# Performance work log

Measured on AMD Instinct MI355X. Metric: run time of the kernel, lower is better.

The kernel has to match this reference:

```python
import jax, jax.numpy as jnp
import numpy as np

B, T, D, H = 2, 2048, 1024, 16
HD = D // H
REG = 16
WIN = 256
ROPE_BASE = 10000.0


def _rope_cos_sin(t, hd):
    theta = 1.0 / (ROPE_BASE ** (jnp.arange(0, hd, 2, dtype=jnp.float32) / hd))  # [hd/2]
    idx_theta = jnp.arange(t, dtype=jnp.float32)[:, None] * theta[None, :]       # [T, hd/2]
    return jnp.cos(idx_theta), jnp.sin(idx_theta)


def _apply_rope(x, cos, sin):
    # x: [B, T, H, HD]
    xs = x.reshape(*x.shape[:-1], HD // 2, 2)
    x0, x1 = xs[..., 0], xs[..., 1]
    c = cos[None, :, None, :]
    s = sin[None, :, None, :]
    out = jnp.stack([x0 * c - x1 * s, x1 * c + x0 * s], axis=-1)
    return out.reshape(x.shape)


def _keep_mask(t):
    # Faithful to _build_attention_register_mask: True = attend (SDPA bool semantics).
    i = jnp.arange(t)[:, None]
    j = jnp.arange(t)[None, :]
    half = WIN // 2
    window_block = (i >= REG) & (j >= jnp.maximum(REG, i - half)) & (j <= i + half)
    blocked = (j < REG) | (i < REG) | window_block
    return ~blocked  # [T, T] bool


def setup_inputs() -> dict:
    key = jax.random.key(0)
    k1, k2, k3 = jax.random.split(key, 3)
    x = jax.random.normal(k1, (B, T, D), dtype=jnp.float32)
    w_attn = jax.random.normal(k2, (3 * D, D), dtype=jnp.float32) * 0.02  # torch Linear weight [out,in]
    w_proj = jax.random.normal(k3, (D, D), dtype=jnp.float32) * 0.02
    return {"x": x, "w_attn": w_attn, "w_proj": w_proj}


def reference(x, w_attn, w_proj):
    b, t, d = x.shape
    qkv = jnp.einsum('btd,ed->bte', x, w_attn)               # [B,T,3D]
    q, k, v = jnp.split(qkv, 3, axis=-1)
    q = q.reshape(b, t, H, HD)
    k = k.reshape(b, t, H, HD)
    v = v.reshape(b, t, H, HD)
    cos, sin = _rope_cos_sin(t, HD)
    q = _apply_rope(q, cos, sin)
    k = _apply_rope(k, cos, sin)
    q = q.transpose(0, 2, 1, 3)  # [B,H,T,HD]
    k = k.transpose(0, 2, 1, 3)
    v = v.transpose(0, 2, 1, 3)
    keep = _keep_mask(t)
    scores = jnp.einsum('bhqd,bhkd->bhqk', q, k) / jnp.sqrt(jnp.float32(HD))
    scores = jnp.where(keep[None, None], scores, -jnp.inf)
    # safe softmax (fully-masked rows -> 0, matching SDPA efficient backends)
    m = jnp.max(scores, axis=-1, keepdims=True)
    m = jnp.where(jnp.isfinite(m), m, 0.0)
    e = jnp.exp(scores - m)
    s = jnp.sum(e, axis=-1, keepdims=True)
    probs = e / jnp.maximum(s, 1e-20)
    y = jnp.einsum('bhqk,bhkd->bhqd', probs, v)
    y = y.transpose(0, 2, 1, 3).reshape(b, t, d)
    return jnp.einsum('btd,ed->bte', y, w_proj)
```

## Files before the change

kernel.cpp:

```cpp
#include <hip/hip_runtime.h>
#include <hip/hip_bf16.h>

#define DEV static __device__ __forceinline__

typedef __attribute__((ext_vector_type(8))) short bf16x8;
typedef __attribute__((ext_vector_type(4))) short bf16x4;
typedef __attribute__((ext_vector_type(4))) float f32x4;

#define MFMA16(a, b, c) __builtin_amdgcn_mfma_f32_16x16x32_bf16((a), (b), (c), 0, 0, 0)

DEV f32x4 pv_mfma(bf16x4 a, bf16x4 b, f32x4 c) {
#if __has_builtin(__builtin_amdgcn_mfma_f32_16x16x16_bf16)
  return __builtin_amdgcn_mfma_f32_16x16x16_bf16(a, b, c, 0, 0, 0);
#elif __has_builtin(__builtin_amdgcn_mfma_f32_16x16x16bf16_1k)
  return __builtin_amdgcn_mfma_f32_16x16x16bf16_1k(a, b, c, 0, 0, 0);
#else
  f32x4 d;
  asm volatile("v_mfma_f32_16x16x16_bf16 %0, %1, %2, %3"
               : "=v"(d) : "v"(a), "v"(b), "v"(c));
  return d;
#endif
}

#define B_ 2
#define T_ 2048
#define D_ 1024
#define H_ 16
#define HD_ 64
#define LOG2E 1.4426950408889634f

DEV short f2bf(float f) {
  union { float f; unsigned u; } w; w.f = f;
  unsigned u = w.u + 0x7fffu + ((w.u >> 16) & 1u);
  return (short)(u >> 16);
}

DEV void gld16(const void* g, void* l) {
  __builtin_amdgcn_global_load_lds(
      (const __attribute__((address_space(1))) void*)g,
      (__attribute__((address_space(3))) void*)l, 16, 0, 0);
}

#define XN 4194304
#define WAN 3145728
__global__ void cvt_k(const float* __restrict__ x, const float* __restrict__ wa,
                      const float* __restrict__ wp, short* __restrict__ xb,
                      short* __restrict__ wab, short* __restrict__ wpb) {
  size_t gi = ((size_t)blockIdx.x * 256 + threadIdx.x) * 8;
  const float* src; short* dst;
  if (gi < XN) { src = x + gi; dst = xb + gi; }
  else if (gi < XN + WAN) { src = wa + (gi - XN); dst = wab + (gi - XN); }
  else { src = wp + (gi - XN - WAN); dst = wpb + (gi - XN - WAN); }
  float4 a = *(const float4*)src;
  float4 b = *(const float4*)(src + 4);
  bf16x8 o;
  o[0] = f2bf(a.x); o[1] = f2bf(a.y); o[2] = f2bf(a.z); o[3] = f2bf(a.w);
  o[4] = f2bf(b.x); o[5] = f2bf(b.y); o[6] = f2bf(b.z); o[7] = f2bf(b.w);
  *(bf16x8*)dst = o;
}

__global__ void rope_table_k(float2* __restrict__ tab) {
  int i = blockIdx.x * 256 + threadIdx.x;
  if (i >= T_ * 32) return;
  int t = i >> 5, d = i & 31;
  float theta = powf(10000.0f, -(float)(2 * d) / 64.0f);
  float a = (float)t * theta;
  tab[i] = make_float2(cosf(a), sinf(a));
}

#define GEMM_CORE(Aptr, Bptr, KDIM)                                              \
  __shared__ short aT[128 * 64];                                                 \
  __shared__ short bT[128 * 64];                                                 \
  const int tid = threadIdx.x;                                                   \
  const int lane = tid & 63, w = tid >> 6;                                       \
  const int l15 = lane & 15, lg = lane >> 4;                                     \
  const int wr = w >> 1, wc = w & 1;                                             \
  const int mBase = blockIdx.y * 128, nBase = blockIdx.x * 128;                  \
  const int lrow = lane >> 3;                                                    \
  const int gch = (lane & 7) ^ lrow;                                             \
  const short* Asrc = (Aptr) + (size_t)(mBase + w * 32 + lrow) * (KDIM) + gch * 8;\
  const short* Bsrc = (Bptr) + (size_t)(nBase + w * 32 + lrow) * (KDIM) + gch * 8;\
  short* aDst = aT + w * 2048;                                                   \
  short* bDst = bT + w * 2048;                                                   \
  f32x4 acc[4][4];                                                               \
  _Pragma("unroll") for (int i = 0; i < 4; ++i)                                  \
  _Pragma("unroll") for (int j = 0; j < 4; ++j)                                  \
      acc[i][j] = (f32x4){0.f, 0.f, 0.f, 0.f};                                   \
  const int nk = (KDIM) / 64;                                                    \
  for (int kt = 0; kt < nk; ++kt) {                                              \
    if (kt) __syncthreads();                                                     \
    _Pragma("unroll") for (int p = 0; p < 4; ++p) {                              \
      gld16(Asrc + kt * 64 + p * 8 * (KDIM), aDst + p * 512);                    \
      gld16(Bsrc + kt * 64 + p * 8 * (KDIM), bDst + p * 512);                    \
    }                                                                            \
    __syncthreads();                \
    bf16x8 af[4][2], bfv[4][2];                                                  \
    _Pragma("unroll") for (int i = 0; i < 4; ++i)                                \
    _Pragma("unroll") for (int s = 0; s < 2; ++s) {                              \
      const int ra = wr * 64 + i * 16 + l15;                                     \
      const int rb = wc * 64 + i * 16 + l15;                                     \
      af[i][s] = *(const bf16x8*)&aT[ra * 64 + (((4 * s + lg) ^ (ra & 7)) * 8)]; \
      bfv[i][s] = *(const bf16x8*)&bT[rb * 64 + (((4 * s + lg) ^ (rb & 7)) * 8)];\
    }                                                                            \
    _Pragma("unroll") for (int mi = 0; mi < 4; ++mi)                             \
    _Pragma("unroll") for (int ni = 0; ni < 4; ++ni)                             \
    _Pragma("unroll") for (int s = 0; s < 2; ++s)                                \
        acc[mi][ni] = MFMA16(af[mi][s], bfv[ni][s], acc[mi][ni]);                \
  }

__global__ void gemm_qkv_k(const short* __restrict__ Xb, const short* __restrict__ Wb,
                           short* __restrict__ Q, short* __restrict__ Ko,
                           short* __restrict__ Vt, const float2* __restrict__ tab) {
  GEMM_CORE(Xb, Wb, 1024)

  const int sec = nBase >> 10;
#pragma unroll
  for (int mi = 0; mi < 4; ++mi) {
    const int m0 = mBase + wr * 64 + mi * 16 + lg * 4;
#pragma unroll
    for (int ni = 0; ni < 4; ++ni) {
      const int n = nBase + wc * 64 + ni * 16 + l15;
      const int hd = n & 63;
      const int h = (n >> 6) & 15;
      if (sec < 2) {
        short* dst = (sec == 0) ? Q : Ko;
        const float qscale = (sec == 0) ? (0.125f * LOG2E) : 1.0f;
#pragma unroll
        for (int r = 0; r < 4; ++r) {
          int m = m0 + r; int b = m >> 11; int t = m & 2047;
          float v = acc[mi][ni][r];
          float pv = __shfl_xor(v, 1);
          float2 cs = tab[t * 32 + (hd >> 1)];
          float o = (lane & 1) ? (v * cs.x + pv * cs.y) : (v * cs.x - pv * cs.y);
          o *= qscale;
          dst[(((size_t)b * H_ + h) * T_ + t) * HD_ + hd] = f2bf(o);
        }
      } else {
        int b = m0 >> 11; int t0 = m0 & 2047;
        short4 s4;
        s4.x = f2bf(acc[mi][ni][0]); s4.y = f2bf(acc[mi][ni][1]);
        s4.z = f2bf(acc[mi][ni][2]); s4.w = f2bf(acc[mi][ni][3]);
        *(short4*)&Vt[(((size_t)b * H_ + h) * HD_ + hd) * T_ + t0] = s4;
      }
    }
  }
}

__global__ __launch_bounds__(256, 4) void attn_k(const short* __restrict__ Qg,
                                                 const short* __restrict__ Kg,
                                                 const short* __restrict__ Vg,
                                                 short* __restrict__ Y) {
  __shared__ short kLds[64 * 72];
  __shared__ short vLds[64 * 72];
  const int tid = threadIdx.x;
  const int lane = tid & 63, w = tid >> 6;
  const int l15 = lane & 15, lg = lane >> 4;
  const int bid = blockIdx.x;
  const int wg = ((bid & 7) << 7) | (bid >> 3);
  const int qt = wg & 31, bh = wg >> 5;
  const int b = bh >> 4, h = bh & 15;
  const int q0 = qt * 64;
  const short* Qh = Qg + (size_t)bh * T_ * HD_;
  const short* Kh = Kg + (size_t)bh * T_ * HD_;
  const short* Vh = Vg + (size_t)bh * HD_ * T_;

  bf16x8 qb[2];
  {
    const int qrow = q0 + w * 16 + l15;
    qb[0] = *(const bf16x8*)&Qh[(size_t)qrow * HD_ + lg * 8];
    qb[1] = *(const bf16x8*)&Qh[(size_t)qrow * HD_ + 32 + lg * 8];
  }
  f32x4 ot[4];
#pragma unroll
  for (int i = 0; i < 4; ++i) ot[i] = (f32x4){0.f, 0.f, 0.f, 0.f};
  float lsum = 0.f;

  const int sRow = tid >> 3, sC = (tid & 7) * 8;
  bf16x8 kreg[2], vreg[2];
  auto issueLoad = [&](int kt) {
    const int k0 = kt * 64;
#pragma unroll
    for (int p = 0; p < 2; ++p) {
      const int row = sRow + p * 32;
      kreg[p] = *(const bf16x8*)&Kh[(size_t)(k0 + row) * HD_ + sC];
      vreg[p] = *(const bf16x8*)&Vh[(size_t)row * T_ + k0 + sC];
    }
  };
  auto inBand = [&](int kt) { const int k0 = kt * 64; return k0 >= q0 - 65 && k0 <= q0 + 65; };

  const int NT = T_ / 64;
  int kt = 0;
  while (kt < NT && inBand(kt)) ++kt;
  issueLoad(kt);

  while (kt < NT) {
    int ktn = kt + 1;
    while (ktn < NT && inBand(ktn)) ++ktn;

    __syncthreads();
#pragma unroll
    for (int p = 0; p < 2; ++p) {
      const int row = sRow + p * 32;
      *(bf16x8*)&kLds[row * 72 + (((tid & 7) ^ (row & 7)) * 8)] = kreg[p];
      *(bf16x8*)&vLds[row * 72 + sC] = vreg[p];
    }
    if (ktn < NT) issueLoad(ktn);
    asm volatile("s_waitcnt lgkmcnt(0)" ::: "memory");
    __builtin_amdgcn_s_barrier();

    const int k0 = kt * 64;
    const bool clean = (q0 >= 16) && (k0 >= 16) &&
                       ((k0 + 63 < q0 - 128) || (k0 > q0 + 63 + 128));

    f32x4 s[4];
#pragma unroll
    for (int i = 0; i < 4; ++i) s[i] = (f32x4){0.f, 0.f, 0.f, 0.f};
    __builtin_amdgcn_s_setprio(1);
#pragma unroll
    for (int nf = 0; nf < 4; ++nf)
#pragma unroll
      for (int ks = 0; ks < 2; ++ks) {
        const int row = nf * 16 + l15;
        bf16x8 ka = *(const bf16x8*)&kLds[row * 72 + (((ks * 4 + lg) ^ (row & 7)) * 8)];
        s[nf] = MFMA16(ka, qb[ks], s[nf]);
      }
    __builtin_amdgcn_s_setprio(0);

    const int i_q = q0 + w * 16 + l15;
    bf16x4 pf[4];
#pragma unroll
    for (int nf = 0; nf < 4; ++nf)
#pragma unroll
      for (int r = 0; r < 4; ++r) {
        if (!clean) {
          const int j = k0 + nf * 16 + lg * 4 + r;
          const bool keep = (i_q >= 16) && (j >= 16) &&
                            ((j < i_q - 128) || (j > i_q + 128));
          if (!keep) s[nf][r] = -__builtin_inff();
        }
        float e = __builtin_amdgcn_exp2f(s[nf][r]);
        lsum += e;
        pf[nf][r] = f2bf(e);
      }

    __builtin_amdgcn_s_setprio(1);
#pragma unroll
    for (int kk = 0; kk < 4; ++kk) {
      bf16x4 va[4];
#pragma unroll
      for (int dt = 0; dt < 4; ++dt)
        va[dt] = *(const bf16x4*)&vLds[(dt * 16 + l15) * 72 + kk * 16 + lg * 4];
#pragma unroll
      for (int dt = 0; dt < 4; ++dt)
        ot[dt] = pv_mfma(va[dt], pf[kk], ot[dt]);
    }
    __builtin_amdgcn_s_setprio(0);
    kt = ktn;
  }

  float l = lsum;
  l += __shfl_xor(l, 16);
  l += __shfl_xor(l, 32);
  const float rl = 1.0f / fmaxf(l, 1e-20f);

  __syncthreads();
  short* tl = kLds + w * (16 * 72);
#pragma unroll
  for (int dt = 0; dt < 4; ++dt) {
    short4 s4;
    s4.x = f2bf(ot[dt][0] * rl);
    s4.y = f2bf(ot[dt][1] * rl);
    s4.z = f2bf(ot[dt][2] * rl);
    s4.w = f2bf(ot[dt][3] * rl);
    *(short4*)&tl[l15 * 72 + dt * 16 + lg * 4] = s4;
  }
  const int rr = lane >> 3, cc = (lane & 7) * 8;
#pragma unroll
  for (int hf = 0; hf < 2; ++hf) {
    const int row = hf * 8 + rr;
    bf16x8 v = *(const bf16x8*)&tl[row * 72 + cc];
    const int t = q0 + w * 16 + row;
    *(bf16x8*)&Y[((size_t)(b * T_ + t)) * D_ + h * HD_ + cc] = v;
  }
}

__global__ void gemm_proj_k(const short* __restrict__ Yg, const short* __restrict__ Wb,
                            float* __restrict__ Out) {
  GEMM_CORE(Yg, Wb, 1024)

#pragma unroll
  for (int mi = 0; mi < 4; ++mi)
#pragma unroll
    for (int ni = 0; ni < 4; ++ni)
#pragma unroll
      for (int r = 0; r < 4; ++r)
        Out[(size_t)(mBase + wr * 64 + mi * 16 + lg * 4 + r) * 1024 +
            nBase + wc * 64 + ni * 16 + l15] = acc[mi][ni][r];
}

extern "C" void kernel_launch(void* const* d_in, const int* in_sizes, int n_in,
                              void* d_out, int out_size, void* d_ws, size_t ws_size,
                              hipStream_t stream) {
  const float* x = (const float*)d_in[0];
  const float* w_attn = (const float*)d_in[1];
  const float* w_proj = (const float*)d_in[2];
  float* out = (float*)d_out;
  char* ws = (char*)d_ws;
  char* outc = (char*)d_out;
  short* Q   = (short*)(ws);
  short* K   = (short*)(ws + (size_t)8388608);
  short* Vt  = (short*)(ws + (size_t)16777216);
  short* Y   = (short*)(ws + (size_t)25165824);
  short* Wpb = (short*)(ws + (size_t)33554432);
  short* Xb   = (short*)(outc);
  short* Wab  = (short*)(outc + (size_t)8388608);
  float2* tab = (float2*)(outc + (size_t)14680064);

  cvt_k<<<dim3(4096), dim3(256), 0, stream>>>(x, w_attn, w_proj, Xb, Wab, Wpb);
  rope_table_k<<<dim3(256), dim3(256), 0, stream>>>(tab);
  gemm_qkv_k<<<dim3(24, 32), dim3(256), 0, stream>>>(Xb, Wab, Q, K, Vt, tab);
  attn_k<<<dim3(B_ * H_ * (T_ / 64)), dim3(256), 0, stream>>>(Q, K, Vt, Y);
  gemm_proj_k<<<dim3(8, 32), dim3(256), 0, stream>>>(Y, Wpb, out);
}
```

Measured before the change: 149.3 us.

## Use packed bf16 convert, raise occupancy bound, drop K LDS swizzle

Replaces the manual round-to-nearest float-to-bf16 conversion of softmax probabilities with the hardware v_cvt_pk_bf16_f32 instruction, packing two values per instruction. Raises the launch-bounds occupancy hint from 4 to 8 blocks per CU, which pushes the compiler toward fewer registers per thread. Also removes the XOR swizzle on K tile LDS stores and reads and uses plain row-major addressing, which could bring back LDS bank conflicts. The tighter register budget risks spills.

```diff
diff --git a/kernel.cpp b/kernel.cpp
--- a/kernel.cpp
+++ b/kernel.cpp
@@ -20,6 +20,15 @@
                : "=v"(d) : "v"(a), "v"(b), "v"(c));
   return d;
 #endif
+}
+
+DEV bf16x4 pk4(float e0, float e1, float e2, float e3) {
+  unsigned lo, hi;
+  asm("v_cvt_pk_bf16_f32 %0, %1, %2" : "=v"(lo) : "v"(e0), "v"(e1));
+  asm("v_cvt_pk_bf16_f32 %0, %1, %2" : "=v"(hi) : "v"(e2), "v"(e3));
+  union { unsigned u[2]; bf16x4 v; } r;
+  r.u[0] = lo; r.u[1] = hi;
+  return r.v;
 }
 
 #define B_ 2
@@ -146,7 +155,7 @@
   }
 }
 
-__global__ __launch_bounds__(256, 4) void attn_k(const short* __restrict__ Qg,
+__global__ __launch_bounds__(256, 8) void attn_k(const short* __restrict__ Qg,
                                                  const short* __restrict__ Kg,
                                                  const short* __restrict__ Vg,
                                                  short* __restrict__ Y) {
@@ -164,12 +173,11 @@
   const short* Kh = Kg + (size_t)bh * T_ * HD_;
   const short* Vh = Vg + (size_t)bh * HD_ * T_;
 
+  const int qrow = q0 + w * 16 + l15;
   bf16x8 qb[2];
-  {
-    const int qrow = q0 + w * 16 + l15;
-    qb[0] = *(const bf16x8*)&Qh[(size_t)qrow * HD_ + lg * 8];
-    qb[1] = *(const bf16x8*)&Qh[(size_t)qrow * HD_ + 32 + lg * 8];
-  }
+  qb[0] = *(const bf16x8*)&Qh[(size_t)qrow * HD_ + lg * 8];
+  qb[1] = *(const bf16x8*)&Qh[(size_t)qrow * HD_ + 32 + lg * 8];
+
   f32x4 ot[4];
 #pragma unroll
   for (int i = 0; i < 4; ++i) ot[i] = (f32x4){0.f, 0.f, 0.f, 0.f};
@@ -200,9 +208,8 @@
     __syncthreads();
 #pragma unroll
     for (int p = 0; p < 2; ++p) {
-      const int row = sRow + p * 32;
-      *(bf16x8*)&kLds[row * 72 + (((tid & 7) ^ (row & 7)) * 8)] = kreg[p];
-      *(bf16x8*)&vLds[row * 72 + sC] = vreg[p];
+      *(bf16x8*)&kLds[(sRow + p * 32) * 72 + sC] = kreg[p];
+      *(bf16x8*)&vLds[(sRow + p * 32) * 72 + sC] = vreg[p];
     }
     if (ktn < NT) issueLoad(ktn);
     asm volatile("s_waitcnt lgkmcnt(0)" ::: "memory");
@@ -220,28 +227,28 @@
     for (int nf = 0; nf < 4; ++nf)
 #pragma unroll
       for (int ks = 0; ks < 2; ++ks) {
-        const int row = nf * 16 + l15;
-        bf16x8 ka = *(const bf16x8*)&kLds[row * 72 + (((ks * 4 + lg) ^ (row & 7)) * 8)];
+        bf16x8 ka = *(const bf16x8*)&kLds[(nf * 16 + l15) * 72 + ks * 32 + lg * 8];
         s[nf] = MFMA16(ka, qb[ks], s[nf]);
       }
     __builtin_amdgcn_s_setprio(0);
 
-    const int i_q = q0 + w * 16 + l15;
     bf16x4 pf[4];
 #pragma unroll
-    for (int nf = 0; nf < 4; ++nf)
+    for (int nf = 0; nf < 4; ++nf) {
+      float e[4];
 #pragma unroll
       for (int r = 0; r < 4; ++r) {
         if (!clean) {
           const int j = k0 + nf * 16 + lg * 4 + r;
-          const bool keep = (i_q >= 16) && (j >= 16) &&
-                            ((j < i_q - 128) || (j > i_q + 128));
+          const bool keep = (qrow >= 16) && (j >= 16) &&
+                            ((j < qrow - 128) || (j > qrow + 128));
           if (!keep) s[nf][r] = -__builtin_inff();
         }
-        float e = __builtin_amdgcn_exp2f(s[nf][r]);
-        lsum += e;
-        pf[nf][r] = f2bf(e);
+        e[r] = __builtin_amdgcn_exp2f(s[nf][r]);
+        lsum += e[r];
       }
+      pf[nf] = pk4(e[0], e[1], e[2], e[3]);
+    }
 
     __builtin_amdgcn_s_setprio(1);
 #pragma unroll
```

Result: slower. 235.7 us (+57.9%).
